# Kernel tuning notes

Measured on AMD Instinct MI355X. Metric: run time of the kernel, lower is better.

The kernel has to match this reference:

```python
import jax, jax.numpy as jnp
import numpy as np

W_WORKERS = 2
Q_LEN = 16
HIDDEN = 4096
N_HEADS = 32
N_KV = 8
HEAD_DIM = 128
L_SHARED = 8192
L_WORKER = 2048
THETA = 10000.0


def rotate_half(x):
    x1, x2 = jnp.split(x, 2, axis=-1)
    return jnp.concatenate((-x2, x1), axis=-1)


def rope_cos_sin(pos):
    # pos: int array [...]; returns cos,sin of shape [..., HEAD_DIM] (HF convention: freqs duplicated)
    inv = 1.0 / (THETA ** (jnp.arange(0, HEAD_DIM, 2, dtype=jnp.float32) / HEAD_DIM))
    ang = pos[..., None].astype(jnp.float32) * inv
    emb = jnp.concatenate((ang, ang), axis=-1)
    return jnp.cos(emb), jnp.sin(emb)


def setup_inputs() -> dict:
    key = jax.random.key(0)
    ks = jax.random.split(key, 16)
    std = 0.02
    # new keys are appended at positions L_WORKER..L_WORKER+Q-1 of each worker's own segment
    pos_new = jnp.broadcast_to(L_WORKER + jnp.arange(Q_LEN), (W_WORKERS, Q_LEN))
    cos_new, sin_new = rope_cos_sin(pos_new)
    return {
        'hidden_states': jax.random.normal(ks[0], (W_WORKERS, Q_LEN, HIDDEN), jnp.float32),
        'Wq': jax.random.normal(ks[1], (N_HEADS * HEAD_DIM, HIDDEN), jnp.float32) * std,
        'bq': jnp.zeros((N_HEADS * HEAD_DIM,), jnp.float32),
        'Wk': jax.random.normal(ks[2], (N_KV * HEAD_DIM, HIDDEN), jnp.float32) * std,
        'bk': jnp.zeros((N_KV * HEAD_DIM,), jnp.float32),
        'Wv': jax.random.normal(ks[3], (N_KV * HEAD_DIM, HIDDEN), jnp.float32) * std,
        'bv': jnp.zeros((N_KV * HEAD_DIM,), jnp.float32),
        'Wo': jax.random.normal(ks[4], (HIDDEN, N_HEADS * HEAD_DIM), jnp.float32) * std,
        'seg_shared_k': jax.random.normal(ks[5], (N_KV, L_SHARED, HEAD_DIM), jnp.float32),
        'seg_shared_v': jax.random.normal(ks[6], (N_KV, L_SHARED, HEAD_DIM), jnp.float32),
        'w0_k': jax.random.normal(ks[7], (N_KV, L_WORKER, HEAD_DIM), jnp.float32),
        'w0_v': jax.random.normal(ks[8], (N_KV, L_WORKER, HEAD_DIM), jnp.float32),
        'w1_k': jax.random.normal(ks[9], (N_KV, L_WORKER, HEAD_DIM), jnp.float32),
        'w1_v': jax.random.normal(ks[10], (N_KV, L_WORKER, HEAD_DIM), jnp.float32),
        'cos_new': cos_new,
        'sin_new': sin_new,
    }


def reference(hidden_states, Wq, bq, Wk, bk, Wv, bv, Wo,
              seg_shared_k, seg_shared_v, w0_k, w0_v, w1_k, w1_v,
              cos_new, sin_new):
    W, Q, _ = hidden_states.shape
    scale = HEAD_DIM ** -0.5
    # projections -> [W, n_heads, Q, D]
    q = (hidden_states @ Wq.T + bq).reshape(W, Q, N_HEADS, HEAD_DIM).transpose(0, 2, 1, 3)
    k_new = (hidden_states @ Wk.T + bk).reshape(W, Q, N_KV, HEAD_DIM).transpose(0, 2, 1, 3)
    v_new = (hidden_states @ Wv.T + bv).reshape(W, Q, N_KV, HEAD_DIM).transpose(0, 2, 1, 3)
    # rope new keys (unsqueeze_dim=1: broadcast over kv heads)
    c, s = cos_new[:, None], sin_new[:, None]
    k_new = k_new * c + rotate_half(k_new) * s
    # cache update: segment 0 = shared prompt, segment 1/2 = worker 0/1 own cache (grows by Q)
    keys = [seg_shared_k,
            jnp.concatenate([w0_k, k_new[0]], axis=1),
            jnp.concatenate([w1_k, k_new[1]], axis=1)]
    values = [seg_shared_v,
              jnp.concatenate([w0_v, v_new[0]], axis=1),
              jnp.concatenate([w1_v, v_new[1]], axis=1)]
    frag_lens = [L_SHARED, L_WORKER + Q, L_WORKER + Q]
    # worker w's view: [shared, other worker's cache, own cache]
    orders = [[0, 2, 1], [0, 1, 2]]
    loc = np.zeros((3, W_WORKERS, Q), dtype=np.int32)
    for w, order in enumerate(orders):
        pos = 0
        for seg in reversed(order):
            pos += frag_lens[seg]
            loc[seg, w] = np.arange(pos - Q, pos)
    loc = jnp.asarray(loc)  # [S, W, Q]
    cos_q, sin_q = rope_cos_sin(loc)  # [S, W, Q, D]
    # hogwild_rope: queries rotated per (segment, worker) location -> [S, W, H, Q, D]
    rq = q[None] * cos_q[:, :, None] + rotate_half(q)[None] * sin_q[:, :, None]
    rep = N_HEADS // N_KV
    scores, v_parts = [], []
    for seg in range(3):
        k_s = jnp.repeat(keys[seg], rep, axis=0)  # GQA expand [H, L_s, D]
        sc = jnp.einsum('whqd,hld->whql', rq[seg], k_s) * scale
        mask = jnp.arange(frag_lens[seg])[None, None, None, :] <= loc[seg][:, None, :, None]
        scores.append(jnp.where(mask, sc, jnp.finfo(sc.dtype).min))
        v_parts.append(jnp.repeat(values[seg], rep, axis=0))
    scores = jnp.concatenate(scores, axis=-1)        # [W, H, Q, Ltot] joint softmax over fragments
    probs = jax.nn.softmax(scores, axis=-1)
    v_all = jnp.concatenate(v_parts, axis=1)         # [H, Ltot, D]
    attn = jnp.einsum('whql,hld->whqd', probs, v_all)
    out = attn.transpose(0, 2, 1, 3).reshape(W, Q, N_HEADS * HEAD_DIM) @ Wo.T
    return out
```

## Files before the change

kernel.cpp:

```cpp
#include <hip/hip_runtime.h>
#include <hip/hip_fp16.h>
#include <cstdint>
#include <cstddef>

#define QL 16
#define LSH 8192
#define LWK 2048
#define SCALE 0.08838834764831845f

typedef __attribute__((ext_vector_type(8))) short short8;
typedef __attribute__((ext_vector_type(4))) short short4v;
typedef __attribute__((ext_vector_type(4))) float f32x4;
typedef __attribute__((ext_vector_type(8))) unsigned short ushort8v;

#if defined(__has_builtin)
#if __has_builtin(__builtin_amdgcn_mfma_f32_16x16x16bf16_1k)
#define HAVE_MFMA16 1
#endif
#endif

__device__ __forceinline__ unsigned short f2bf(float f) {
  unsigned int u = __float_as_uint(f);
  u += 0x7fffu + ((u >> 16) & 1u);
  return (unsigned short)(u >> 16);
}
__device__ __forceinline__ float bf2f(unsigned short b) {
  return __uint_as_float(((unsigned int)b) << 16);
}

__device__ __forceinline__ void gload_lds16(const float* g, float* lds) {
  __builtin_amdgcn_global_load_lds(
      (const __attribute__((address_space(1))) void*)g,
      (__attribute__((address_space(3))) void*)lds, 16, 0, 0);
}

__global__ __launch_bounds__(256) void k_cast(
    const float* __restrict__ in, unsigned short* __restrict__ outp, int n4)
{
  int i = blockIdx.x * 256 + threadIdx.x;
  if (i < n4) {
    float4 v = ((const float4*)in)[i];
    ushort4 p; p.x = f2bf(v.x); p.y = f2bf(v.y); p.z = f2bf(v.z); p.w = f2bf(v.w);
    ((ushort4*)outp)[i] = p;
  }
}

__global__ __launch_bounds__(256) void k_gemm4(
    const unsigned short* __restrict__ Xbf,
    const float* __restrict__ W0, const float* __restrict__ W1, const float* __restrict__ W2,
    const float* __restrict__ b0, const float* __restrict__ b1, const float* __restrict__ b2,
    float* __restrict__ outA, float* __restrict__ outB, int Ntot)
{
  __shared__ float Ws[16 * 516];
  const int bx = blockIdx.x;
  const int n0 = (bx >> 1) * 16;
  const int khalf = bx & 1;
  const float* W; const float* bias; int row0;
  if (n0 < 4096)      { W = W0; bias = b0; row0 = n0; }
  else if (n0 < 5120) { W = W1; bias = b1; row0 = n0 - 4096; }
  else                { W = W2; bias = b2; row0 = n0 - 5120; }
  const int t = threadIdx.x;
  const int w_id = t >> 6;
  const int lane = t & 63;
  const int l15 = lane & 15;
  const int quad = lane >> 4;
  const int cb0 = khalf * 2048;

  f32x4 C0 = {0.f,0.f,0.f,0.f}, C1 = {0.f,0.f,0.f,0.f};

  for (int c = 0; c < 4; ++c) {
    const int cbase = cb0 + c * 512;
    __syncthreads();
#pragma unroll
    for (int i = 0; i < 8; ++i) {
      int idx = w_id * 8 + i;
      int r = idx >> 1, hh = idx & 1;
      const float* g = W + (size_t)(row0 + r) * 4096 + cbase + hh * 256 + lane * 4;
      gload_lds16(g, &Ws[r * 516 + hh * 256]);
    }
    __syncthreads();
    const int wk = w_id * 128;
#pragma unroll
    for (int ks = 0; ks < 4; ++ks) {
      int ko = wk + ks * 32 + quad * 8;
      f32x4 wlo = *(const f32x4*)(&Ws[l15 * 516 + ko]);
      f32x4 whi = *(const f32x4*)(&Ws[l15 * 516 + ko + 4]);
      short8 bfr;
      bfr[0] = (short)f2bf(wlo[0]); bfr[1] = (short)f2bf(wlo[1]);
      bfr[2] = (short)f2bf(wlo[2]); bfr[3] = (short)f2bf(wlo[3]);
      bfr[4] = (short)f2bf(whi[0]); bfr[5] = (short)f2bf(whi[1]);
      bfr[6] = (short)f2bf(whi[2]); bfr[7] = (short)f2bf(whi[3]);
      short8 a0 = *(const short8*)(Xbf + (size_t)l15 * 4096 + cbase + ko);
      short8 a1 = *(const short8*)(Xbf + (size_t)(16 + l15) * 4096 + cbase + ko);
      C0 = __builtin_amdgcn_mfma_f32_16x16x32_bf16(a0, bfr, C0, 0, 0, 0);
      C1 = __builtin_amdgcn_mfma_f32_16x16x32_bf16(a1, bfr, C1, 0, 0, 0);
    }
  }
  __syncthreads();
  float* Red = Ws;
#pragma unroll
  for (int i = 0; i < 4; ++i) {
    Red[w_id * 512 + (quad * 4 + i) * 16 + l15] = C0[i];
    Red[w_id * 512 + 256 + (quad * 4 + i) * 16 + l15] = C1[i];
  }
  __syncthreads();
  float* dst = khalf ? outB : outA;
#pragma unroll
  for (int e = t; e < 512; e += 256) {
    float s = Red[e] + Red[512 + e] + Red[1024 + e] + Red[1536 + e];
    int m = e >> 4, n = e & 15;
    if (khalf == 0 && bias) s += bias[row0 + n];
    dst[(size_t)m * Ntot + n0 + n] = s;
  }
}

__global__ __launch_bounds__(256) void k_add(
    const float* __restrict__ A, const float* __restrict__ B,
    float* __restrict__ o, int n4)
{
  int i = blockIdx.x * 256 + threadIdx.x;
  if (i < n4) {
    float4 a = ((const float4*)A)[i], b = ((const float4*)B)[i];
    float4 r; r.x = a.x + b.x; r.y = a.y + b.y; r.z = a.z + b.z; r.w = a.w + b.w;
    ((float4*)o)[i] = r;
  }
}

__global__ __launch_bounds__(256) void k_rope(
    const float* __restrict__ qA, const float* __restrict__ qB,
    const float* __restrict__ cosn, const float* __restrict__ sinn,
    unsigned short* __restrict__ rq, unsigned short* __restrict__ knew,
    unsigned short* __restrict__ vnew)
{
  const int g = blockIdx.x * 256 + threadIdx.x;
  const float LOGTH = 9.210340371976184f;
  if (g < 393216) {
    int d = g & 127, q = (g >> 7) & 15, head = (g >> 11) & 31, w = (g >> 16) & 1, var = g >> 17;
    int tok = w * 16 + q;
    int col = head * 128 + d;
    size_t ix = (size_t)tok * 6144 + col;
    float val = qA[ix] + qB[ix];
    size_t ir = (d < 64) ? ix + 64 : ix - 64;
    float rot = qA[ir] + qB[ir];
    if (d < 64) rot = -rot;
    int pos = (var == 0 ? 12304 : (var == 1 ? 4112 : 2048)) + q;
    int i = d & 63;
    float inv = expf(-(float)i * (LOGTH / 64.0f));
    float ang = (float)pos * inv;
    float c = cosf(ang), s = sinf(ang);
    rq[g] = f2bf((val * c + rot * s) * SCALE);
  } else {
    int g2 = g - 393216;
    if (g2 < 65536) {
      int isv = (g2 >= 32768);
      if (isv) g2 -= 32768;
      int d = g2 & 127, q = (g2 >> 7) & 15, h = (g2 >> 11) & 7, w = (g2 >> 14) & 1;
      int tok = w * 16 + q;
      if (isv) {
        size_t ix = (size_t)tok * 6144 + 5120 + h * 128 + d;
        vnew[g2] = f2bf(qA[ix] + qB[ix]);
      } else {
        size_t ix = (size_t)tok * 6144 + 4096 + h * 128 + d;
        float val = qA[ix] + qB[ix];
        size_t ir = (d < 64) ? ix + 64 : ix - 64;
        float rot = qA[ir] + qB[ir];
        if (d < 64) rot = -rot;
        float c = cosn[tok * 128 + d], s = sinn[tok * 128 + d];
        knew[g2] = f2bf(val * c + rot * s);
      }
    }
  }
}

__global__ __launch_bounds__(256, 2) void k_attn(
    const float* __restrict__ shk, const float* __restrict__ shv,
    const float* __restrict__ w0k, const float* __restrict__ w0v,
    const float* __restrict__ w1k, const float* __restrict__ w1v,
    const unsigned short* __restrict__ rq,
    const unsigned short* __restrict__ knew, const unsigned short* __restrict__ vnew,
    __half* __restrict__ accP, float* __restrict__ lP)
{
  __shared__ alignas(16) unsigned short Ks[64 * 136];
  __shared__ alignas(16) unsigned short Vts[128 * 72];
#ifndef HAVE_MFMA16
  __shared__ alignas(16) unsigned short Plds[4 * 32 * 72];
#endif

  const int h = blockIdx.x / 50;
  const int cidx = blockIdx.x % 50;
  int kind, k0, nk; bool is_new;
  if (cidx < 32)      { kind = 0; k0 = cidx * 256; nk = 256; is_new = false; }
  else if (cidx < 41) { int c = cidx - 32; kind = 1; k0 = c * 256; nk = (c == 8) ? 16 : 256; is_new = (c == 8); }
  else                { int c = cidx - 41; kind = 2; k0 = c * 256; nk = (c == 8) ? 16 : 256; is_new = (c == 8); }

  const int t = threadIdx.x;
  const int w_id = t >> 6;
  const int lane = t & 63;
  const int l15 = lane & 15;
  const int quad = lane >> 4;
  const int worker = w_id >> 1;
  const int headpair = w_id & 1;
  const int tg = t >> 7;
  const int dv = t & 127;
  const int rbase = t >> 5;
  const int doff = (t & 31) * 4;

  int var; bool causal;
  if (kind == 0)      { var = 0; causal = false; }
  else if (kind == 1) { var = (worker == 0) ? 2 : 1; causal = (worker == 0); }
  else                { var = (worker == 1) ? 2 : 1; causal = (worker == 1); }

  const float* Ksrc = (kind == 0) ? (shk + (size_t)h * LSH * 128)
                     : (kind == 1) ? (w0k + (size_t)h * LWK * 128)
                                   : (w1k + (size_t)h * LWK * 128);
  const float* Vsrc = (kind == 0) ? (shv + (size_t)h * LSH * 128)
                     : (kind == 1) ? (w0v + (size_t)h * LWK * 128)
                                   : (w1v + (size_t)h * LWK * 128);
  const int wseg = (kind == 2) ? 1 : 0;
  const unsigned short* knsrc = knew + ((size_t)wseg * 8 + h) * 16 * 128;
  const unsigned short* vnsrc = vnew + ((size_t)wseg * 8 + h) * 16 * 128;

  short8 arq[2][4];
#pragma unroll
  for (int mt = 0; mt < 2; ++mt) {
    int head = h * 4 + headpair * 2 + mt;
    const unsigned short* base =
        rq + ((((size_t)var * 2 + worker) * 32 + head) * 16 + l15) * 128 + quad * 8;
#pragma unroll
    for (int ks = 0; ks < 4; ++ks) arq[mt][ks] = *(const short8*)(base + ks * 32);
  }

  float lrow[2] = {0.f, 0.f};
  f32x4 acc[2][8];
#pragma unroll
  for (int mt = 0; mt < 2; ++mt)
#pragma unroll
    for (int dt = 0; dt < 8; ++dt) acc[mt][dt] = {0.f,0.f,0.f,0.f};

  float4 kf[8];
  float  vf[32];

  auto load_tile = [&](int st) {
    const int kb = k0 + st * 64;
    if (!is_new) {
#pragma unroll
      for (int rd = 0; rd < 8; ++rd)
        kf[rd] = *(const float4*)(Ksrc + (size_t)(kb + rd * 8 + rbase) * 128 + doff);
#pragma unroll
      for (int g = 0; g < 4; ++g)
#pragma unroll
        for (int i = 0; i < 8; ++i)
          vf[g * 8 + i] = Vsrc[(size_t)(kb + (tg + g * 2) * 8 + i) * 128 + dv];
    } else {
#pragma unroll
      for (int rd = 0; rd < 8; ++rd) {
        ushort4 p = *(const ushort4*)(knsrc + (size_t)((rd * 8 + rbase) & 15) * 128 + doff);
        kf[rd].x = bf2f(p.x); kf[rd].y = bf2f(p.y);
        kf[rd].z = bf2f(p.z); kf[rd].w = bf2f(p.w);
      }
#pragma unroll
      for (int g = 0; g < 4; ++g)
#pragma unroll
        for (int i = 0; i < 8; ++i)
          vf[g * 8 + i] = bf2f(vnsrc[(size_t)(((tg + g * 2) * 8 + i) & 15) * 128 + dv]);
    }
  };

  const int nst = (nk + 63) >> 6;
  load_tile(0);

  for (int st = 0; st < nst; ++st) {
    __syncthreads();
#pragma unroll
    for (int rd = 0; rd < 8; ++rd) {
      ushort4 p; p.x = f2bf(kf[rd].x); p.y = f2bf(kf[rd].y);
      p.z = f2bf(kf[rd].z); p.w = f2bf(kf[rd].w);
      *(ushort4*)(&Ks[(rd * 8 + rbase) * 136 + doff]) = p;
    }
#pragma unroll
    for (int g = 0; g < 4; ++g) {
      ushort8v p;
#pragma unroll
      for (int i = 0; i < 8; ++i) p[i] = f2bf(vf[g * 8 + i]);
      *(ushort8v*)(&Vts[dv * 72 + (tg + g * 2) * 8]) = p;
    }
    __syncthreads();
    if (st + 1 < nst) load_tile(st + 1);

#ifdef HAVE_MFMA16
    short4v pv[2][4];
#endif
#pragma unroll
    for (int mt = 0; mt < 2; ++mt) {
      f32x4 S[4];
#pragma unroll
      for (int nt = 0; nt < 4; ++nt) S[nt] = {0.f,0.f,0.f,0.f};
#pragma unroll
      for (int ks = 0; ks < 4; ++ks)
#pragma unroll
        for (int nt = 0; nt < 4; ++nt) {
          short8 kfr = *(const short8*)(&Ks[(nt * 16 + l15) * 136 + ks * 32 + quad * 8]);
          S[nt] = __builtin_amdgcn_mfma_f32_16x16x32_bf16(kfr, arq[mt][ks], S[nt], 0, 0, 0);
        }
      if (is_new) {
#pragma unroll
        for (int nt = 0; nt < 4; ++nt)
#pragma unroll
          for (int i = 0; i < 4; ++i) {
            int loc = st * 64 + nt * 16 + quad * 4 + i;
            if (loc >= nk || (causal && loc > l15)) S[nt][i] = -3.0e38f;
          }
      }
      float rs = 0.0f;
#pragma unroll
      for (int nt = 0; nt < 4; ++nt)
#pragma unroll
        for (int i = 0; i < 4; ++i) {
          float p = __expf(fminf(S[nt][i], 60.0f));
          S[nt][i] = p;
          rs += p;
        }
#ifdef HAVE_MFMA16
#pragma unroll
      for (int nt = 0; nt < 4; ++nt) {
        short4v pp;
        pp[0] = (short)f2bf(S[nt][0]); pp[1] = (short)f2bf(S[nt][1]);
        pp[2] = (short)f2bf(S[nt][2]); pp[3] = (short)f2bf(S[nt][3]);
        pv[mt][nt] = pp;
      }
#else
#pragma unroll
      for (int nt = 0; nt < 4; ++nt)
#pragma unroll
        for (int i = 0; i < 4; ++i)
          Plds[w_id * (32 * 72) + (mt * 16 + l15) * 72 + nt * 16 + quad * 4 + i] =
              f2bf(S[nt][i]);
#endif
      rs += __shfl_xor(rs, 16, 64);
      rs += __shfl_xor(rs, 32, 64);
      lrow[mt] += rs;
    }
#ifdef HAVE_MFMA16
#pragma unroll
    for (int dt = 0; dt < 8; ++dt)
#pragma unroll
      for (int kc = 0; kc < 4; ++kc) {
        short4v vfr = *(const short4v*)(&Vts[(dt * 16 + l15) * 72 + kc * 16 + quad * 4]);
        acc[0][dt] = __builtin_amdgcn_mfma_f32_16x16x16bf16_1k(pv[0][kc], vfr, acc[0][dt], 0, 0, 0);
        acc[1][dt] = __builtin_amdgcn_mfma_f32_16x16x16bf16_1k(pv[1][kc], vfr, acc[1][dt], 0, 0, 0);
      }
#else
    short8 ap[2][2];
#pragma unroll
    for (int mt = 0; mt < 2; ++mt)
#pragma unroll
      for (int ks2 = 0; ks2 < 2; ++ks2)
        ap[mt][ks2] = *(const short8*)(
            &Plds[w_id * (32 * 72) + (mt * 16 + l15) * 72 + ks2 * 32 + quad * 8]);
#pragma unroll
    for (int dt = 0; dt < 8; ++dt)
#pragma unroll
      for (int ks2 = 0; ks2 < 2; ++ks2) {
        short8 vfr = *(const short8*)(&Vts[(dt * 16 + l15) * 72 + ks2 * 32 + quad * 8]);
        acc[0][dt] = __builtin_amdgcn_mfma_f32_16x16x32_bf16(ap[0][ks2], vfr, acc[0][dt], 0, 0, 0);
        acc[1][dt] = __builtin_amdgcn_mfma_f32_16x16x32_bf16(ap[1][ks2], vfr, acc[1][dt], 0, 0, 0);
      }
#endif
  }

  __half* accB = accP + (size_t)blockIdx.x * 128 * 128;
#pragma unroll
  for (int mt = 0; mt < 2; ++mt)
#pragma unroll
    for (int dt = 0; dt < 8; ++dt)
#pragma unroll
      for (int i = 0; i < 4; ++i) {
        int row = w_id * 32 + mt * 16 + quad * 4 + i;
        int d = dt * 16 + l15;
        accB[row * 128 + d] = __float2half(acc[mt][dt][i]);
      }
  if (quad == 0) {
#pragma unroll
    for (int mt = 0; mt < 2; ++mt) {
      int row = w_id * 32 + mt * 16 + l15;
      lP[(size_t)blockIdx.x * 128 + row] = lrow[mt];
    }
  }
}

__global__ __launch_bounds__(128) void k_combine(
    const __half* __restrict__ accP, const float* __restrict__ lP,
    unsigned short* __restrict__ attnX)
{
  __shared__ float sl[50];
  const int h = blockIdx.x >> 7;
  const int r = blockIdx.x & 127;
  const int d = threadIdx.x;
  if (d < 50) sl[d] = lP[(size_t)(h * 50 + d) * 128 + r];
  __syncthreads();
  float L = 0.0f, A = 0.0f;
#pragma unroll
  for (int c = 0; c < 50; ++c) L += sl[c];
#pragma unroll
  for (int cc = 0; cc < 50; cc += 10) {
    float p[10];
#pragma unroll
    for (int i = 0; i < 10; ++i)
      p[i] = __half2float(accP[((size_t)(h * 50 + cc + i) * 128 + r) * 128 + d]);
#pragma unroll
    for (int i = 0; i < 10; ++i) A += p[i];
  }
  int workerv = r >> 6, headpairv = (r >> 5) & 1, mtv = (r >> 4) & 1, q = r & 15;
  int head = h * 4 + headpairv * 2 + mtv;
  attnX[(size_t)(workerv * 16 + q) * 4096 + head * 128 + d] = f2bf(A / L);
}

extern "C" void kernel_launch(void* const* d_in, const int* in_sizes, int n_in,
                              void* d_out, int out_size, void* d_ws, size_t ws_size,
                              hipStream_t stream)
{
  const float* hs   = (const float*)d_in[0];
  const float* Wq   = (const float*)d_in[1];
  const float* bq   = (const float*)d_in[2];
  const float* Wk   = (const float*)d_in[3];
  const float* bk   = (const float*)d_in[4];
  const float* Wv   = (const float*)d_in[5];
  const float* bv   = (const float*)d_in[6];
  const float* Wo   = (const float*)d_in[7];
  const float* shk  = (const float*)d_in[8];
  const float* shv  = (const float*)d_in[9];
  const float* w0k  = (const float*)d_in[10];
  const float* w0v  = (const float*)d_in[11];
  const float* w1k  = (const float*)d_in[12];
  const float* w1v  = (const float*)d_in[13];
  const float* cosn = (const float*)d_in[14];
  const float* sinn = (const float*)d_in[15];
  float* out = (float*)d_out;

  char* ws = (char*)d_ws;
  float*          qkvA   = (float*)(ws + 0);
  unsigned short* rq     = (unsigned short*)(ws + 786432);
  unsigned short* knew   = (unsigned short*)(ws + 1572864);
  unsigned short* vnew   = (unsigned short*)(ws + 1638400);
  unsigned short* hsbf   = (unsigned short*)(ws + 1703936);
  unsigned short* attnXb = (unsigned short*)(ws + 1966080);
  float*          lP     = (float*)(ws + 2228224);
  __half*         accP   = (__half*)(ws + 2433024);
  float*          qkvB   = (float*)(ws + 15540224);
  float*          outA   = (float*)(ws + 2433024);
  float*          outB   = (float*)(ws + 2433024 + 786432);

  k_cast<<<128, 256, 0, stream>>>(hs, hsbf, 32768);
  k_gemm4<<<768, 256, 0, stream>>>(hsbf, Wq, Wk, Wv, bq, bk, bv, qkvA, qkvB, 6144);
  k_rope<<<1792, 256, 0, stream>>>(qkvA, qkvB, cosn, sinn, rq, knew, vnew);
  k_attn<<<400, 256, 0, stream>>>(shk, shv, w0k, w0v, w1k, w1v, rq, knew, vnew, accP, lP);
  k_combine<<<1024, 128, 0, stream>>>(accP, lP, attnXb);
  k_gemm4<<<512, 256, 0, stream>>>(attnXb, Wo, Wo, Wo, nullptr, nullptr, nullptr, outA, outB, 4096);
  k_add<<<192, 256, 0, stream>>>(outA, outB, out, 49152);
}
```

Before: 302.4 us.

## Use 512-thread attention blocks with one 16-row query tile per wave

Doubles the attention block from 4 to 8 waves, so each wave handles one head's 16 query rows instead of two. The cooperative K/V tile loads are split over 512 threads, which halves each thread's prefetch registers. The aim is more waves in flight to hide global-memory latency on the streaming KV reads. In exchange every wave now reloads the K fragments from LDS for its own single query tile, which doubles LDS traffic per tile, and the launch bound of 512 threads with 2 blocks per CU limits registers per thread.

```diff
diff --git a/kernel.cpp b/kernel.cpp
--- a/kernel.cpp
+++ b/kernel.cpp
@@ -172,7 +172,7 @@
   }
 }
 
-__global__ __launch_bounds__(256, 2) void k_attn(
+__global__ __launch_bounds__(512, 2) void k_attn(
     const float* __restrict__ shk, const float* __restrict__ shv,
     const float* __restrict__ w0k, const float* __restrict__ w0v,
     const float* __restrict__ w1k, const float* __restrict__ w1v,
@@ -183,7 +183,7 @@
   __shared__ alignas(16) unsigned short Ks[64 * 136];
   __shared__ alignas(16) unsigned short Vts[128 * 72];
 #ifndef HAVE_MFMA16
-  __shared__ alignas(16) unsigned short Plds[4 * 32 * 72];
+  __shared__ alignas(16) unsigned short Plds[8 * 16 * 72];
 #endif
 
   const int h = blockIdx.x / 50;
@@ -198,12 +198,12 @@
   const int lane = t & 63;
   const int l15 = lane & 15;
   const int quad = lane >> 4;
-  const int worker = w_id >> 1;
-  const int headpair = w_id & 1;
+  const int worker = w_id >> 2;
+  const int hq = w_id & 3;
+  const int col4 = t & 31;
+  const int rowb = t >> 5;
+  const int dv = t & 127;
   const int tg = t >> 7;
-  const int dv = t & 127;
-  const int rbase = t >> 5;
-  const int doff = (t & 31) * 4;
 
   int var; bool causal;
   if (kind == 0)      { var = 0; causal = false; }
@@ -220,49 +220,46 @@
   const unsigned short* knsrc = knew + ((size_t)wseg * 8 + h) * 16 * 128;
   const unsigned short* vnsrc = vnew + ((size_t)wseg * 8 + h) * 16 * 128;
 
-  short8 arq[2][4];
-#pragma unroll
-  for (int mt = 0; mt < 2; ++mt) {
-    int head = h * 4 + headpair * 2 + mt;
+  const int head = h * 4 + hq;
+  short8 arq[4];
+  {
     const unsigned short* base =
         rq + ((((size_t)var * 2 + worker) * 32 + head) * 16 + l15) * 128 + quad * 8;
 #pragma unroll
-    for (int ks = 0; ks < 4; ++ks) arq[mt][ks] = *(const short8*)(base + ks * 32);
-  }
-
-  float lrow[2] = {0.f, 0.f};
-  f32x4 acc[2][8];
-#pragma unroll
-  for (int mt = 0; mt < 2; ++mt)
-#pragma unroll
-    for (int dt = 0; dt < 8; ++dt) acc[mt][dt] = {0.f,0.f,0.f,0.f};
-
-  float4 kf[8];
-  float  vf[32];
+    for (int ks = 0; ks < 4; ++ks) arq[ks] = *(const short8*)(base + ks * 32);
+  }
+
+  float lrow = 0.f;
+  f32x4 acc[8];
+#pragma unroll
+  for (int dt = 0; dt < 8; ++dt) acc[dt] = {0.f,0.f,0.f,0.f};
+
+  float4 kf[4];
+  float  vf[16];
 
   auto load_tile = [&](int st) {
     const int kb = k0 + st * 64;
     if (!is_new) {
 #pragma unroll
-      for (int rd = 0; rd < 8; ++rd)
-        kf[rd] = *(const float4*)(Ksrc + (size_t)(kb + rd * 8 + rbase) * 128 + doff);
-#pragma unroll
-      for (int g = 0; g < 4; ++g)
+      for (int i = 0; i < 4; ++i)
+        kf[i] = *(const float4*)(Ksrc + (size_t)(kb + i * 16 + rowb) * 128 + col4 * 4);
+#pragma unroll
+      for (int g = 0; g < 2; ++g)
 #pragma unroll
         for (int i = 0; i < 8; ++i)
-          vf[g * 8 + i] = Vsrc[(size_t)(kb + (tg + g * 2) * 8 + i) * 128 + dv];
+          vf[g * 8 + i] = Vsrc[(size_t)(kb + g * 32 + tg * 8 + i) * 128 + dv];
     } else {
 #pragma unroll
-      for (int rd = 0; rd < 8; ++rd) {
-        ushort4 p = *(const ushort4*)(knsrc + (size_t)((rd * 8 + rbase) & 15) * 128 + doff);
-        kf[rd].x = bf2f(p.x); kf[rd].y = bf2f(p.y);
-        kf[rd].z = bf2f(p.z); kf[rd].w = bf2f(p.w);
-      }
-#pragma unroll
-      for (int g = 0; g < 4; ++g)
+      for (int i = 0; i < 4; ++i) {
+        ushort4 p = *(const ushort4*)(knsrc + (size_t)((i * 16 + rowb) & 15) * 128 + col4 * 4);
+        kf[i].x = bf2f(p.x); kf[i].y = bf2f(p.y);
+        kf[i].z = bf2f(p.z); kf[i].w = bf2f(p.w);
+      }
+#pragma unroll
+      for (int g = 0; g < 2; ++g)
 #pragma unroll
         for (int i = 0; i < 8; ++i)
-          vf[g * 8 + i] = bf2f(vnsrc[(size_t)(((tg + g * 2) * 8 + i) & 15) * 128 + dv]);
+          vf[g * 8 + i] = bf2f(vnsrc[(size_t)((g * 32 + tg * 8 + i) & 15) * 128 + dv]);
     }
   };
 
@@ -272,119 +269,106 @@
   for (int st = 0; st < nst; ++st) {
     __syncthreads();
 #pragma unroll
-    for (int rd = 0; rd < 8; ++rd) {
-      ushort4 p; p.x = f2bf(kf[rd].x); p.y = f2bf(kf[rd].y);
-      p.z = f2bf(kf[rd].z); p.w = f2bf(kf[rd].w);
-      *(ushort4*)(&Ks[(rd * 8 + rbase) * 136 + doff]) = p;
-    }
-#pragma unroll
-    for (int g = 0; g < 4; ++g) {
+    for (int i = 0; i < 4; ++i) {
+      ushort4 p; p.x = f2bf(kf[i].x); p.y = f2bf(kf[i].y);
+      p.z = f2bf(kf[i].z); p.w = f2bf(kf[i].w);
+      *(ushort4*)(&Ks[(i * 16 + rowb) * 136 + col4 * 4]) = p;
+    }
+#pragma unroll
+    for (int g = 0; g < 2; ++g) {
       ushort8v p;
 #pragma unroll
       for (int i = 0; i < 8; ++i) p[i] = f2bf(vf[g * 8 + i]);
-      *(ushort8v*)(&Vts[dv * 72 + (tg + g * 2) * 8]) = p;
+      *(ushort8v*)(&Vts[dv * 72 + (g * 4 + tg) * 8]) = p;
     }
     __syncthreads();
     if (st + 1 < nst) load_tile(st + 1);
 
+    f32x4 S[4];
+#pragma unroll
+    for (int nt = 0; nt < 4; ++nt) S[nt] = {0.f,0.f,0.f,0.f};
+#pragma unroll
+    for (int ks = 0; ks < 4; ++ks)
+#pragma unroll
+      for (int nt = 0; nt < 4; ++nt) {
+        short8 kfr = *(const short8*)(&Ks[(nt * 16 + l15) * 136 + ks * 32 + quad * 8]);
+        S[nt] = __builtin_amdgcn_mfma_f32_16x16x32_bf16(kfr, arq[ks], S[nt], 0, 0, 0);
+      }
+    if (is_new) {
+#pragma unroll
+      for (int nt = 0; nt < 4; ++nt)
+#pragma unroll
+        for (int i = 0; i < 4; ++i) {
+          int loc = st * 64 + nt * 16 + quad * 4 + i;
+          if (loc >= nk || (causal && loc > l15)) S[nt][i] = -3.0e38f;
+        }
+    }
+    float rs = 0.0f;
+#pragma unroll
+    for (int nt = 0; nt < 4; ++nt)
+#pragma unroll
+      for (int i = 0; i < 4; ++i) {
+        float p = __expf(fminf(S[nt][i], 60.0f));
+        S[nt][i] = p;
+        rs += p;
+      }
 #ifdef HAVE_MFMA16
-    short4v pv[2][4];
+    short4v pv[4];
+#pragma unroll
+    for (int nt = 0; nt < 4; ++nt) {
+      short4v pp;
+      pp[0] = (short)f2bf(S[nt][0]); pp[1] = (short)f2bf(S[nt][1]);
+      pp[2] = (short)f2bf(S[nt][2]); pp[3] = (short)f2bf(S[nt][3]);
+      pv[nt] = pp;
+    }
+#else
+#pragma unroll
+    for (int nt = 0; nt < 4; ++nt)
+#pragma unroll
+      for (int i = 0; i < 4; ++i)
+        Plds[w_id * (16 * 72) + l15 * 72 + nt * 16 + quad * 4 + i] = f2bf(S[nt][i]);
 #endif
-#pragma unroll
-    for (int mt = 0; mt < 2; ++mt) {
-      f32x4 S[4];
-#pragma unroll
-      for (int nt = 0; nt < 4; ++nt) S[nt] = {0.f,0.f,0.f,0.f};
-#pragma unroll
-      for (int ks = 0; ks < 4; ++ks)
-#pragma unroll
-        for (int nt = 0; nt < 4; ++nt) {
-          short8 kfr = *(const short8*)(&Ks[(nt * 16 + l15) * 136 + ks * 32 + quad * 8]);
-          S[nt] = __builtin_amdgcn_mfma_f32_16x16x32_bf16(kfr, arq[mt][ks], S[nt], 0, 0, 0);
-        }
-      if (is_new) {
-#pragma unroll
-        for (int nt = 0; nt < 4; ++nt)
-#pragma unroll
-          for (int i = 0; i < 4; ++i) {
-            int loc = st * 64 + nt * 16 + quad * 4 + i;
-            if (loc >= nk || (causal && loc > l15)) S[nt][i] = -3.0e38f;
-          }
-      }
-      float rs = 0.0f;
-#pragma unroll
-      for (int nt = 0; nt < 4; ++nt)
-#pragma unroll
-        for (int i = 0; i < 4; ++i) {
-          float p = __expf(fminf(S[nt][i], 60.0f));
-          S[nt][i] = p;
-          rs += p;
-        }
-#ifdef HAVE_MFMA16
-#pragma unroll
-      for (int nt = 0; nt < 4; ++nt) {
-        short4v pp;
-        pp[0] = (short)f2bf(S[nt][0]); pp[1] = (short)f2bf(S[nt][1]);
-        pp[2] = (short)f2bf(S[nt][2]); pp[3] = (short)f2bf(S[nt][3]);
-        pv[mt][nt] = pp;
-      }
-#else
-#pragma unroll
-      for (int nt = 0; nt < 4; ++nt)
-#pragma unroll
-        for (int i = 0; i < 4; ++i)
-          Plds[w_id * (32 * 72) + (mt * 16 + l15) * 72 + nt * 16 + quad * 4 + i] =
-              f2bf(S[nt][i]);
-#endif
-      rs += __shfl_xor(rs, 16, 64);
-      rs += __shfl_xor(rs, 32, 64);
-      lrow[mt] += rs;
-    }
+    rs += __shfl_xor(rs, 16, 64);
+    rs += __shfl_xor(rs, 32, 64);
+    lrow += rs;
+
 #ifdef HAVE_MFMA16
 #pragma unroll
     for (int dt = 0; dt < 8; ++dt)
 #pragma unroll
       for (int kc = 0; kc < 4; ++kc) {
         short4v vfr = *(const short4v*)(&Vts[(dt * 16 + l15) * 72 + kc * 16 + quad * 4]);
-        acc[0][dt] = __builtin_amdgcn_mfma_f32_16x16x16bf16_1k(pv[0][kc], vfr, acc[0][dt], 0, 0, 0);
-        acc[1][dt] = __builtin_amdgcn_mfma_f32_16x16x16bf16_1k(pv[1][kc], vfr, acc[1][dt], 0, 0, 0);
+        acc[dt] = __builtin_amdgcn_mfma_f32_16x16x16bf16_1k(pv[kc], vfr, acc[dt], 0, 0, 0);
       }
 #else
-    short8 ap[2][2];
-#pragma unroll
-    for (int mt = 0; mt < 2; ++mt)
-#pragma unroll
-      for (int ks2 = 0; ks2 < 2; ++ks2)
-        ap[mt][ks2] = *(const short8*)(
-            &Plds[w_id * (32 * 72) + (mt * 16 + l15) * 72 + ks2 * 32 + quad * 8]);
+    short8 ap[2];
+#pragma unroll
+    for (int ks2 = 0; ks2 < 2; ++ks2)
+      ap[ks2] = *(const short8*)(
+          &Plds[w_id * (16 * 72) + l15 * 72 + ks2 * 32 + quad * 8]);
 #pragma unroll
     for (int dt = 0; dt < 8; ++dt)
 #pragma unroll
       for (int ks2 = 0; ks2 < 2; ++ks2) {
         short8 vfr = *(const short8*)(&Vts[(dt * 16 + l15) * 72 + ks2 * 32 + quad * 8]);
-        acc[0][dt] = __builtin_amdgcn_mfma_f32_16x16x32_bf16(ap[0][ks2], vfr, acc[0][dt], 0, 0, 0);
-        acc[1][dt] = __builtin_amdgcn_mfma_f32_16x16x32_bf16(ap[1][ks2], vfr, acc[1][dt], 0, 0, 0);
+        acc[dt] = __builtin_amdgcn_mfma_f32_16x16x32_bf16(ap[ks2], vfr, acc[dt], 0, 0, 0);
       }
 #endif
   }
 
   __half* accB = accP + (size_t)blockIdx.x * 128 * 128;
-#pragma unroll
-  for (int mt = 0; mt < 2; ++mt)
-#pragma unroll
-    for (int dt = 0; dt < 8; ++dt)
-#pragma unroll
-      for (int i = 0; i < 4; ++i) {
-        int row = w_id * 32 + mt * 16 + quad * 4 + i;
-        int d = dt * 16 + l15;
-        accB[row * 128 + d] = __float2half(acc[mt][dt][i]);
-      }
+  const int wrow = worker * 64 + hq * 16;
+#pragma unroll
+  for (int dt = 0; dt < 8; ++dt)
+#pragma unroll
+    for (int i = 0; i < 4; ++i) {
+      int row = wrow + quad * 4 + i;
+      int d = dt * 16 + l15;
+      accB[row * 128 + d] = __float2half(acc[dt][i]);
+    }
   if (quad == 0) {
-#pragma unroll
-    for (int mt = 0; mt < 2; ++mt) {
-      int row = w_id * 32 + mt * 16 + l15;
-      lP[(size_t)blockIdx.x * 128 + row] = lrow[mt];
-    }
+    int row = wrow + l15;
+    lP[(size_t)blockIdx.x * 128 + row] = lrow;
   }
 }
 
@@ -453,7 +437,7 @@
   k_cast<<<128, 256, 0, stream>>>(hs, hsbf, 32768);
   k_gemm4<<<768, 256, 0, stream>>>(hsbf, Wq, Wk, Wv, bq, bk, bv, qkvA, qkvB, 6144);
   k_rope<<<1792, 256, 0, stream>>>(qkvA, qkvB, cosn, sinn, rq, knew, vnew);
-  k_attn<<<400, 256, 0, stream>>>(shk, shv, w0k, w0v, w1k, w1v, rq, knew, vnew, accP, lP);
+  k_attn<<<400, 512, 0, stream>>>(shk, shv, w0k, w0v, w1k, w1v, rq, knew, vnew, accP, lP);
   k_combine<<<1024, 128, 0, stream>>>(accP, lP, attnXb);
   k_gemm4<<<512, 256, 0, stream>>>(attnXb, Wo, Wo, Wo, nullptr, nullptr, nullptr, outA, outB, 4096);
   k_add<<<192, 256, 0, stream>>>(outA, outB, out, 49152);
```

Measured after the change: 296.8 us. No clear change (-1.9%).
